# Performance work log

Hardware: AMD Instinct MI355X
Metric: run time of the kernel (lower is better)

The kernel has to match this reference:

```python
import jax, jax.numpy as jnp
import numpy as np
import jax.scipy.linalg as jsl

N_SAMPLES = 100000
N_COMPONENTS = 64
N_FEATURES = 32
LOW, HIGH = -0.1, 0.1


def setup_inputs() -> dict:
    key = jax.random.key(0)
    k_x, k_mu = jax.random.split(key)
    X = jax.random.normal(k_x, (N_SAMPLES, N_FEATURES), dtype=jnp.float32)
    means = jax.random.uniform(k_mu, (N_COMPONENTS, N_FEATURES),
                               minval=LOW, maxval=HIGH, dtype=jnp.float32)
    # torch init: stack of tril(eye(D)) == identity for each component
    eye = jnp.eye(N_FEATURES, dtype=jnp.float32)
    scale_tril = jnp.tile(eye[None, :, :], (N_COMPONENTS, 1, 1))
    log_weights = jnp.zeros((N_COMPONENTS,), dtype=jnp.float32)
    return {"X": X, "means": means, "scale_tril": scale_tril,
            "log_weights": log_weights}


def reference(X, means, scale_tril, log_weights):
    N, D = X.shape
    LOG_2PI = jnp.log(jnp.asarray(2.0 * np.pi, dtype=X.dtype))

    def comp_log_prob(mu, L):
        # MVN log-prob via triangular whitening (matches torch MVN(scale_tril=L))
        diff = (X - mu).T                     # [D, N]
        z = jsl.solve_triangular(L, diff, lower=True)  # [D, N]
        maha = jnp.sum(z * z, axis=0)          # [N]
        half_logdet = jnp.sum(jnp.log(jnp.diagonal(L)))
        return -0.5 * (D * LOG_2PI + maha) - half_logdet  # [N]

    logp = jax.vmap(comp_log_prob)(means, scale_tril)  # [K, N]

    # E-step: responsibilities (raw exp, as in the original; no logsumexp)
    weights = jax.nn.softmax(log_weights)              # [K]
    unnorm = weights[:, None] * jnp.exp(logp)          # [K, N]
    resp = unnorm / jnp.sum(unnorm, axis=0, keepdims=True)  # [K, N]

    # M-step: note torch's F.log_softmax(log_weights[k], dim=-1) on a 0-d
    # tensor is identically 0 (softmax of a single element), so it is omitted.
    log_likelihood = jnp.sum(resp * logp, axis=0)      # [N]
    return -jnp.mean(log_likelihood)
```

## Files before the change

### kernel.cpp

```cpp
#include <hip/hip_runtime.h>
#include <math.h>

#define NS 100000
#define NC 64
#define ND 32
#define NK 576
#define NBLK ((NS + 255) / 256)
#define QBYTES (NC * NK * 2)
#define NCPB 8
#define LOG2PI 1.8378770664093453f

typedef __attribute__((ext_vector_type(8))) __bf16 bf16x8;
typedef __attribute__((ext_vector_type(8))) float  floatx8;
typedef __attribute__((ext_vector_type(4))) float  floatx4;



template<int I, int Q>
__device__ __forceinline__ void load_row(const floatx4* ls4, floatx4 (&rb)[8]) {
    if constexpr (Q <= I / 4) {
        rb[Q] = ls4[I * 8 + Q];
        load_row<I, Q + 1>(ls4, rb);
    }
}

template<int I, int L>
__device__ __forceinline__ void fchain(const floatx4 (&rb)[8], const float (&a)[ND], float& s) {
    if constexpr (L < I) {
        s = fmaf(-rb[L / 4][L % 4], a[L], s);
        fchain<I, L + 1>(rb, a, s);
    }
}

template<int I>
__device__ __forceinline__ void fsub2(const floatx4* ls4, float (&a)[ND], int j) {
    if constexpr (I < ND) {
        floatx4 rb[8];
        load_row<I, 0>(ls4, rb);
        float s = (I == j) ? 1.0f : 0.0f;
        fchain<I, 0>(rb, a, s);
        float v = s / rb[I / 4][I % 4];
        a[I] = (I < j) ? 0.0f : v;
        fsub2<I + 1>(ls4, a, j);
    }
}

template<int Q>
__device__ __forceinline__ void store_ac(float* acrow, const float (&a)[ND]) {
    if constexpr (Q < 8) {
        floatx4 t;
        t[0] = a[4 * Q + 0]; t[1] = a[4 * Q + 1];
        t[2] = a[4 * Q + 2]; t[3] = a[4 * Q + 3];
        *(floatx4*)(acrow + 4 * Q) = t;
        store_ac<Q + 1>(acrow, a);
    }
}

template<int JJ>
__device__ __forceinline__ void qpack(bf16x8& v, const float* Pc, const float* bbc,
                                      int t, int quad) {
    if constexpr (JJ < 8) {
        int u = quad * 8 + JJ;
        float val;
        if (t == 0)       val = -0.5f * Pc[u * 32 + u];
        else if (t < 16)  val = -Pc[u * 32 + ((u + t) & 31)];
        else if (t == 16) val = (u < 16) ? -Pc[u * 32 + u + 16] : bbc[u - 16];
        else              val = (u < 16) ? bbc[16 + u] : 0.0f;
        v[JJ] = (__bf16)val;
        qpack<JJ + 1>(v, Pc, bbc, t, quad);
    }
}

__launch_bounds__(512)
__global__ void gmm_setup(const float* __restrict__ means,
                          const float* __restrict__ scale_tril,
                          const float* __restrict__ log_weights,
                          __bf16* __restrict__ Qf,
                          float* __restrict__ lw,
                          float* __restrict__ kc,
                          float* __restrict__ out) {
    __shared__ __align__(16) floatx4 LsP4[NCPB * 256];
    __shared__ __align__(16) float Ac[NCPB][32][36];
    __shared__ float mu_s[NCPB][32];
    __shared__ float bb_s[NCPB][32];

    const int tid  = threadIdx.x;
    const int b    = blockIdx.x;
    const int w    = tid >> 6;
    const int lane = tid & 63;

    if (b == 0 && tid == 0) out[0] = 0.0f;

    {
        const floatx4* g4 = (const floatx4*)scale_tril + (size_t)b * 2048;
#pragma unroll
        for (int q = 0; q < 4; ++q)
            LsP4[q * 512 + tid] = g4[q * 512 + tid];
        if (tid < NCPB * 32)
            mu_s[tid >> 5][tid & 31] = means[(size_t)(b * NCPB + (tid >> 5)) * ND + (tid & 31)];
    }
    __syncthreads();

    const floatx4* ls4 = LsP4 + w * 256;
    if (lane < ND) {
        float a[ND];
        fsub2<0>(ls4, a, lane);
        store_ac<0>(&Ac[w][lane][0], a);
    }
    float hv = (lane < ND) ? logf(((const float*)LsP4)[w * 1024 + lane * 33]) : 0.0f;
#pragma unroll
    for (int off = 1; off < 64; off <<= 1) hv += __shfl_xor(hv, off);
    float hld = hv;
    __syncthreads();

    {
        int c = tid >> 6, half = (tid >> 5) & 1, i = tid & 31;
        const floatx4* rI4 = (const floatx4*)&Ac[c][i][0];
        float* Pc = (float*)LsP4 + c * 1024;
        for (int j16 = 0; j16 < 16; ++j16) {
            int j = half * 16 + j16;
            const floatx4* rJ4 = (const floatx4*)&Ac[c][j][0];
            float s = 0.0f;
#pragma unroll
            for (int q = 0; q < 8; ++q) {
                floatx4 x = rI4[q], y = rJ4[q];
                s = fmaf(x[0], y[0], s); s = fmaf(x[1], y[1], s);
                s = fmaf(x[2], y[2], s); s = fmaf(x[3], y[3], s);
            }
            Pc[i * 32 + j] = s;
        }
    }
    __syncthreads();

    const float* Pw = (const float*)LsP4 + w * 1024;
    float bbv = 0.0f;
    if (lane < ND) {
        for (int j = 0; j < ND; ++j) bbv = fmaf(Pw[lane * 32 + j], mu_s[w][j], bbv);
        bb_s[w][lane] = bbv;
    }
    float ccv = (lane < ND) ? mu_s[w][lane] * bbv : 0.0f;
#pragma unroll
    for (int off = 1; off < 64; off <<= 1) ccv += __shfl_xor(ccv, off);
    int comp = b * NCPB + w;
    if (lane == 0)
        kc[comp] = -0.5f * ccv - 16.0f * LOG2PI - hld;

    if (b == 0 && w == 0) {
        float x = log_weights[lane];
        float mx = x;
#pragma unroll
        for (int off = 1; off < 64; off <<= 1) mx = fmaxf(mx, __shfl_xor(mx, off));
        float e = __expf(x - mx);
#pragma unroll
        for (int off = 1; off < 64; off <<= 1) e += __shfl_xor(e, off);
        lw[lane] = x - mx - logf(e);
    }

    {
        int mt = comp >> 4, colk = comp & 15;
        const float* bbc = &bb_s[w][0];
        bf16x8* qdst = (bf16x8*)Qf;
        {
            int t = lane >> 2, quad = lane & 3;
            bf16x8 v;
            qpack<0>(v, Pw, bbc, t, quad);
            qdst[(size_t)(mt * 18 + t) * 64 + quad * 16 + colk] = v;
        }
        if (lane < 8) {
            int cl2 = 64 + lane;
            int t = cl2 >> 2, quad = cl2 & 3;
            bf16x8 v;
            qpack<0>(v, Pw, bbc, t, quad);
            qdst[(size_t)(mt * 18 + t) * 64 + quad * 16 + colk] = v;
        }
    }
}


template<int G>
__device__ __forceinline__ void fill_x(const float4* p, float (&xr)[ND], int quad) {
    if constexpr (G < 8) {
        float4 v = p[(G + 2 * quad) & 7];
        xr[4 * G + 0] = v.x; xr[4 * G + 1] = v.y;
        xr[4 * G + 2] = v.z; xr[4 * G + 3] = v.w;
        fill_x<G + 1>(p, xr, quad);
    }
}

template<int T, int JJ>
__device__ __forceinline__ void feat(const float (&xr0)[ND], const float (&xr1)[ND],
                                     int quad, floatx8& f0, floatx8& f1) {
    if constexpr (JJ < 8) {
        float a0, a1, b0, b1;
        if constexpr (T < 16) {
            a0 = xr0[JJ]; b0 = xr0[(JJ + T) & 31];
            a1 = xr1[JJ]; b1 = xr1[(JJ + T) & 31];
        } else if constexpr (T == 16) {
            a0 = (quad < 2) ? xr0[JJ] : 1.0f;  b0 = xr0[(JJ + 16) & 31];
            a1 = (quad < 2) ? xr1[JJ] : 1.0f;  b1 = xr1[(JJ + 16) & 31];
        } else {
            a0 = (quad < 2) ? xr0[(JJ + 16) & 31] : 0.0f; b0 = 1.0f;
            a1 = (quad < 2) ? xr1[(JJ + 16) & 31] : 0.0f; b1 = 1.0f;
        }
        f0[JJ] = a0 * b0;
        f1[JJ] = a1 * b1;
        feat<T, JJ + 1>(xr0, xr1, quad, f0, f1);
    }
}

template<int T, int MT>
__device__ __forceinline__ void mfma_step(const unsigned char* qlane, bf16x8 b0, bf16x8 b1,
                                          floatx4 (&A0)[4], floatx4 (&A1)[4]) {
    if constexpr (MT < 4) {
        bf16x8 af = *(const bf16x8*)(qlane + (MT * 18 + T) * 1024);
        A0[MT] = __builtin_amdgcn_mfma_f32_16x16x32_bf16(af, b0, A0[MT], 0, 0, 0);
        A1[MT] = __builtin_amdgcn_mfma_f32_16x16x32_bf16(af, b1, A1[MT], 0, 0, 0);
        mfma_step<T, MT + 1>(qlane, b0, b1, A0, A1);
    }
}

template<int T>
__device__ __forceinline__ void kloop(const unsigned char* qlane,
                                      const float (&xr0)[ND], const float (&xr1)[ND],
                                      int quad, floatx4 (&A0)[4], floatx4 (&A1)[4]) {
    if constexpr (T < 18) {
        floatx8 f0, f1;
        feat<T, 0>(xr0, xr1, quad, f0, f1);
        bf16x8 b0 = __builtin_convertvector(f0, bf16x8);
        bf16x8 b1 = __builtin_convertvector(f1, bf16x8);
        mfma_step<T, 0>(qlane, b0, b1, A0, A1);
        kloop<T + 1>(qlane, xr0, xr1, quad, A0, A1);
    }
}

template<int MT, int R>
__device__ __forceinline__ void epi_r(const floatx4 (&A0)[4], const floatx4 (&A1)[4],
                                      floatx4 lwv, floatx4 kcv,
                                      float& s0, float& w0, float& s1, float& w1) {
    if constexpr (R < 4) {
        float lp0 = A0[MT][R] + kcv[R];
        float e0 = __expf(lp0 + lwv[R]);
        s0 += e0; w0 = fmaf(e0, lp0, w0);
        float lp1 = A1[MT][R] + kcv[R];
        float e1 = __expf(lp1 + lwv[R]);
        s1 += e1; w1 = fmaf(e1, lp1, w1);
        epi_r<MT, R + 1>(A0, A1, lwv, kcv, s0, w0, s1, w1);
    }
}

template<int MT>
__device__ __forceinline__ void epi(const float* lw_s, const float* kc_s, int quad,
                                    const floatx4 (&A0)[4], const floatx4 (&A1)[4],
                                    float& s0, float& w0, float& s1, float& w1) {
    if constexpr (MT < 4) {
        floatx4 lwv = *(const floatx4*)&lw_s[MT * 16 + quad * 4];
        floatx4 kcv = *(const floatx4*)&kc_s[MT * 16 + quad * 4];
        epi_r<MT, 0>(A0, A1, lwv, kcv, s0, w0, s1, w1);
        epi<MT + 1>(lw_s, kc_s, quad, A0, A1, s0, w0, s1, w1);
    }
}

__device__ __forceinline__ float pair_ll(const float* __restrict__ X,
                                         const unsigned char* qlane,
                                         const float* lw_s, const float* kc_s,
                                         int n0, int quad) {
    int n1 = n0 + 16;
    int n0c = n0 < NS ? n0 : NS - 1;
    int n1c = n1 < NS ? n1 : NS - 1;

    float xr0[ND], xr1[ND];
    fill_x<0>((const float4*)(X + (size_t)n0c * ND), xr0, quad);
    fill_x<0>((const float4*)(X + (size_t)n1c * ND), xr1, quad);

    floatx4 A0[4], A1[4];
#pragma unroll
    for (int mt = 0; mt < 4; ++mt) {
        A0[mt] = (floatx4){0.f, 0.f, 0.f, 0.f};
        A1[mt] = (floatx4){0.f, 0.f, 0.f, 0.f};
    }

    kloop<0>(qlane, xr0, xr1, quad, A0, A1);

    float s0 = 0.f, w0 = 0.f, s1 = 0.f, w1 = 0.f;
    epi<0>(lw_s, kc_s, quad, A0, A1, s0, w0, s1, w1);

    s0 += __shfl_xor(s0, 16); s0 += __shfl_xor(s0, 32);
    w0 += __shfl_xor(w0, 16); w0 += __shfl_xor(w0, 32);
    s1 += __shfl_xor(s1, 16); s1 += __shfl_xor(s1, 32);
    w1 += __shfl_xor(w1, 16); w1 += __shfl_xor(w1, 32);

    float ll = 0.0f;
    ll += (n0 < NS) ? (w0 / s0) : 0.0f;
    ll += (n1 < NS) ? (w1 / s1) : 0.0f;
    return ll;
}

__launch_bounds__(256, 2)
__global__ void gmm_main(const float* __restrict__ X,
                         const __bf16* __restrict__ Qf,
                         const float* __restrict__ lw,
                         const float* __restrict__ kc,
                         float* __restrict__ out) {
    __shared__ __align__(16) unsigned char qlds[QBYTES];
    __shared__ float lw_s[NC];
    __shared__ float kc_s[NC];
    __shared__ float partial[4];
    int tid = threadIdx.x;
    if (tid < NC) { lw_s[tid] = lw[tid]; kc_s[tid] = kc[tid]; }
    {
        const float4* gsrc = (const float4*)Qf;
        float4* ldst = (float4*)qlds;
#pragma unroll
        for (int i = 0; i < QBYTES / 16 / 256; ++i)
            ldst[i * 256 + tid] = gsrc[i * 256 + tid];
    }
    __syncthreads();

    const int lane = tid & 63;
    const int wave = tid >> 6;
    const int quad = lane >> 4;
    const unsigned char* qlane = qlds + lane * 16;

    int base = blockIdx.x * 256 + wave * 32 + (lane & 15);

    float ll = pair_ll(X, qlane, lw_s, kc_s, base, quad);
    asm volatile("" ::: "memory");
    ll      += pair_ll(X, qlane, lw_s, kc_s, base + 128, quad);

#pragma unroll
    for (int off = 1; off < 64; off <<= 1) ll += __shfl_xor(ll, off);
    if (lane == 0) partial[wave] = ll * 0.25f;
    __syncthreads();

    if (tid == 0) {
        float blk = partial[0] + partial[1] + partial[2] + partial[3];
        atomicAdd(out, blk * (-1.0f / (float)NS));
    }
}

extern "C" void kernel_launch(void* const* d_in, const int* in_sizes, int n_in,
                              void* d_out, int out_size, void* d_ws, size_t ws_size,
                              hipStream_t stream) {
    const float* X           = (const float*)d_in[0];
    const float* means       = (const float*)d_in[1];
    const float* scale_tril  = (const float*)d_in[2];
    const float* log_weights = (const float*)d_in[3];

    char* ws = (char*)d_ws;
    __bf16* Qf = (__bf16*)ws;
    float*  lw = (float*)(ws + 73728);
    float*  kc = (float*)(ws + 73984);

    gmm_setup<<<NC / NCPB, 512, 0, stream>>>(means, scale_tril, log_weights,
                                             Qf, lw, kc, (float*)d_out);
    gmm_main<<<NBLK, 256, 0, stream>>>(X, Qf, lw, kc, (float*)d_out);
}
```

Measured before the change: 93.19 us.

## Launch fixed 512-block grid with per-wave unit scheduling and early X prefetch

```diff
diff --git a/kernel.cpp b/kernel.cpp
--- a/kernel.cpp
+++ b/kernel.cpp
@@ -5,10 +5,14 @@
 #define NC 64
 #define ND 32
 #define NK 576
-#define NBLK ((NS + 255) / 256)
 #define QBYTES (NC * NK * 2)
 #define NCPB 8
 #define LOG2PI 1.8378770664093453f
+
+#define MBLK 512
+#define NWAVES (MBLK * 4)
+#define NUNITS (NS / 32)
+#define SECOND (NUNITS - NWAVES)
 
 typedef __attribute__((ext_vector_type(8))) __bf16 bf16x8;
 typedef __attribute__((ext_vector_type(8))) float  floatx8;
@@ -260,18 +264,10 @@
     }
 }
 
-__device__ __forceinline__ float pair_ll(const float* __restrict__ X,
-                                         const unsigned char* qlane,
+__device__ __forceinline__ float unit_ll(const unsigned char* qlane,
                                          const float* lw_s, const float* kc_s,
-                                         int n0, int quad) {
-    int n1 = n0 + 16;
-    int n0c = n0 < NS ? n0 : NS - 1;
-    int n1c = n1 < NS ? n1 : NS - 1;
-
-    float xr0[ND], xr1[ND];
-    fill_x<0>((const float4*)(X + (size_t)n0c * ND), xr0, quad);
-    fill_x<0>((const float4*)(X + (size_t)n1c * ND), xr1, quad);
-
+                                         const float (&xr0)[ND], const float (&xr1)[ND],
+                                         int quad) {
     floatx4 A0[4], A1[4];
 #pragma unroll
     for (int mt = 0; mt < 4; ++mt) {
@@ -289,10 +285,7 @@
     s1 += __shfl_xor(s1, 16); s1 += __shfl_xor(s1, 32);
     w1 += __shfl_xor(w1, 16); w1 += __shfl_xor(w1, 32);
 
-    float ll = 0.0f;
-    ll += (n0 < NS) ? (w0 / s0) : 0.0f;
-    ll += (n1 < NS) ? (w1 / s1) : 0.0f;
-    return ll;
+    return w0 / s0 + w1 / s1;
 }
 
 __launch_bounds__(256, 2)
@@ -306,6 +299,17 @@
     __shared__ float kc_s[NC];
     __shared__ float partial[4];
     int tid = threadIdx.x;
+
+    const int lane = tid & 63;
+    const int wave = tid >> 6;
+    const int quad = lane >> 4;
+    const int g    = blockIdx.x * 4 + wave;
+
+    int n0 = g * 32 + (lane & 15);
+    float xr0[ND], xr1[ND];
+    fill_x<0>((const float4*)(X + (size_t)n0 * ND), xr0, quad);
+    fill_x<0>((const float4*)(X + (size_t)(n0 + 16) * ND), xr1, quad);
+
     if (tid < NC) { lw_s[tid] = lw[tid]; kc_s[tid] = kc[tid]; }
     {
         const float4* gsrc = (const float4*)Qf;
@@ -316,16 +320,18 @@
     }
     __syncthreads();
 
-    const int lane = tid & 63;
-    const int wave = tid >> 6;
-    const int quad = lane >> 4;
     const unsigned char* qlane = qlds + lane * 16;
 
-    int base = blockIdx.x * 256 + wave * 32 + (lane & 15);
-
-    float ll = pair_ll(X, qlane, lw_s, kc_s, base, quad);
-    asm volatile("" ::: "memory");
-    ll      += pair_ll(X, qlane, lw_s, kc_s, base + 128, quad);
+    float ll = unit_ll(qlane, lw_s, kc_s, xr0, xr1, quad);
+
+    if (g < SECOND) {
+        asm volatile("" ::: "memory");
+        int n0b = (g + NWAVES) * 32 + (lane & 15);
+        float yr0[ND], yr1[ND];
+        fill_x<0>((const float4*)(X + (size_t)n0b * ND), yr0, quad);
+        fill_x<0>((const float4*)(X + (size_t)(n0b + 16) * ND), yr1, quad);
+        ll += unit_ll(qlane, lw_s, kc_s, yr0, yr1, quad);
+    }
 
 #pragma unroll
     for (int off = 1; off < 64; off <<= 1) ll += __shfl_xor(ll, off);
@@ -353,5 +359,5 @@
 
     gmm_setup<<<NC / NCPB, 512, 0, stream>>>(means, scale_tril, log_weights,
                                              Qf, lw, kc, (float*)d_out);
-    gmm_main<<<NBLK, 256, 0, stream>>>(X, Qf, lw, kc, (float*)d_out);
-}
+    gmm_main<<<MBLK, 256, 0, stream>>>(X, Qf, lw, kc, (float*)d_out);
+}
```

After: 95.71 us. 2.7% more time.
